# Performance work log

Measured on AMD Instinct MI355X. Metric: run time of the kernel, lower is better.

## Reference

```python
import jax, jax.numpy as jnp
import numpy as np

B, H, L, DM = 16, 8, 512, 512
DK = DM // H  # 64
POW = 2


def setup_inputs() -> dict:
    rng = jax.random.key(0)
    ks = jax.random.split(rng, 16)
    s = 0.05
    d = {
        "query": jax.random.normal(ks[0], (B, L, DM), jnp.float32),
        "key": jax.random.normal(ks[1], (B, L, DM), jnp.float32),
        "value": jax.random.normal(ks[2], (B, L, DM), jnp.float32),
        # torch nn.Linear weights: [out_features, in_features]
        "Wq": jax.random.normal(ks[3], (DM, DM), jnp.float32) * s,
        "bq": jax.random.normal(ks[4], (DM,), jnp.float32) * s,
        "Wk": jax.random.normal(ks[5], (DM, DM), jnp.float32) * s,
        "bk": jax.random.normal(ks[6], (DM,), jnp.float32) * s,
        "Wv": jax.random.normal(ks[7], (DM, DM), jnp.float32) * s,
        "bv": jax.random.normal(ks[8], (DM,), jnp.float32) * s,
        # FCgamma: d_k -> 2 (LrMo == 2)
        "Wg": jax.random.normal(ks[9], (2, DK), jnp.float32) * s,
        "bg": jnp.full((2,), 0.05, jnp.float32),
        "lam1": jnp.zeros((1,), jnp.float32),
        "Wo": jax.random.normal(ks[10], (DM, DM), jnp.float32) * s,
        "bo": jax.random.normal(ks[11], (DM,), jnp.float32) * s,
    }
    return d


def reference(query, key, value, Wq, bq, Wk, bk, Wv, bv, Wg, bg, lam1, Wo, bo):
    def proj(x, W, b):
        # (B,L,DM) -> (B,H,L,DK)
        return (x @ W.T + b).reshape(B, L, H, DK).transpose(0, 2, 1, 3)

    q = proj(query, Wq, bq)
    k = proj(key, Wk, bk)
    v = proj(value, Wv, bv)

    # NOTE: original code overwrites the scaled scores with unscaled QK^T
    scores = jnp.einsum('bhqd,bhkd->bhqk', q, k)  # [B,H,L,L]
    attn = jax.nn.softmax(scores, axis=-1)

    # LrMo == 2: per-row gammas from FCgamma(q) -> 2 channels
    g = q @ Wg.T + bg                      # [B,H,L,2]
    qp = (jnp.abs(g) + 1.0) ** (-POW)      # (|g|+1)^(-pow)

    t = jnp.arange(L, dtype=jnp.float32)
    dist = -0.5 * (t[:, None] - t[None, :]) ** 2   # dist[i,j] = -(i-j)^2/2
    tril = jnp.tril(dist, -1)
    triu = jnp.triu(dist, 0)
    # diag_embed(v) @ M == row-scaling v[i]*M[i,:]
    adj = jnp.exp(qp[..., 1][..., None] * tril + qp[..., 0][..., None] * triu)

    # max-normalize rows of attn
    attn = attn / jnp.max(attn, axis=-1, keepdims=True)
    # sigmoid-gated mix with distance adjacency
    sg = jax.nn.sigmoid(lam1)  # shape (1,)
    attn = sg * attn + (1.0 - sg) * adj
    # degree (row-sum) normalization, non-symmetric
    attn = attn / (jnp.sum(attn, axis=-1, keepdims=True) + 1e-9)

    out = jnp.einsum('bhqk,bhkd->bhqd', attn, v)
    out = out.transpose(0, 2, 1, 3).reshape(B, L, DM)
    return out @ Wo.T + bo
```

## Files before the change

kernel.cpp:

```cpp
#include <hip/hip_runtime.h>
#include <hip/hip_fp16.h>
#include <math.h>

#define B_  16
#define H_  8
#define L_  512
#define DM_ 512
#define DK_ 64
#define LOG2E_ 1.44269504088896340736f
#define NLOG2E_H_ 0.72134752044f

typedef _Float16 f16;
typedef __attribute__((ext_vector_type(2)))  __fp16   fp16v2;
typedef __attribute__((ext_vector_type(8)))  _Float16 f16x8;
typedef __attribute__((ext_vector_type(16))) float f32x16;

__device__ __forceinline__ unsigned pkrtz(float a, float b) {
    union { fp16v2 v; unsigned u; } cv;
    cv.v = __builtin_amdgcn_cvt_pkrtz(a, b);
    return cv.u;
}
__device__ __forceinline__ void plswap(unsigned &x, unsigned &y) {
    asm("v_permlane32_swap_b32 %0, %1" : "+v"(x), "+v"(y));
}

__global__ __launch_bounds__(256) void convw_pack(
    const float* __restrict__ Wq, const float* __restrict__ Wk,
    const float* __restrict__ Wv, const float* __restrict__ Wo,
    f16* __restrict__ Wpk)
{
    const float* src[4] = {Wq, Wk, Wv, Wo};
    const int t = blockIdx.x * 256 + threadIdx.x;
    const int m    = t >> 15;
    const int r    = t & 32767;
    const int lane = r & 31;
    const int hf   = (r >> 5) & 1;
    const int ks   = (r >> 6) & 31;
    const int nb   = r >> 11;
    const float* p = src[m] + (size_t)(nb * 32 + lane) * 512 + ks * 16 + hf * 8;
    float4 x0 = *(const float4*)(p);
    float4 x1 = *(const float4*)(p + 4);
    uint4 v;
    v.x = pkrtz(x0.x, x0.y); v.y = pkrtz(x0.z, x0.w);
    v.z = pkrtz(x1.x, x1.y); v.w = pkrtz(x1.z, x1.w);
    *(uint4*)&Wpk[(size_t)m * 262144 + (size_t)r * 8] = v;
}

template<int XF16, int OUTF32, int TRANSOUT, int NWAVES, int NT>
__device__ __forceinline__ void gemm_stream_core(
    const void* __restrict__ Xv, const f16* __restrict__ Wpk_m,
    const float* __restrict__ bias, void* __restrict__ Yv,
    int row0, int col0, f16* Xl)
{
    const int tid   = threadIdx.x;
    const int w     = tid >> 6;
    const int lane  = tid & 63;
    const int lq    = lane & 31;
    const int half_ = lane >> 5;
    const int colw  = col0 + w * (NT * 32);

    {
        constexpr int TPR = NWAVES * 64 / 32;
        constexpr int FPT = 512 / TPR;
        const int r = tid / TPR, s = tid % TPR;
        const unsigned swz = (r & 7) << 4;
        if (XF16) {
            const f16* X = (const f16*)Xv + (size_t)(row0 + r) * 512 + s * FPT;
            #pragma unroll
            for (int j = 0; j < FPT / 8; ++j) {
                uint4 v = *(const uint4*)(X + j * 8);
                *(uint4*)((char*)Xl + ((r * 1024 + s * FPT * 2 + j * 16) ^ swz)) = v;
            }
        } else {
            const float* X = (const float*)Xv + (size_t)(row0 + r) * 512 + s * FPT;
            #pragma unroll
            for (int j = 0; j < FPT / 8; ++j) {
                float4 x0 = *(const float4*)(X + j * 8);
                float4 x1 = *(const float4*)(X + j * 8 + 4);
                uint4 v;
                v.x = pkrtz(x0.x, x0.y); v.y = pkrtz(x0.z, x0.w);
                v.z = pkrtz(x1.x, x1.y); v.w = pkrtz(x1.z, x1.w);
                *(uint4*)((char*)Xl + ((r * 1024 + s * FPT * 2 + j * 16) ^ swz)) = v;
            }
        }
    }
    __syncthreads();

    f32x16 acc[NT];
    #pragma unroll
    for (int nt = 0; nt < NT; ++nt)
        #pragma unroll
        for (int i = 0; i < 16; ++i) acc[nt][i] = 0.f;

    const f16* wp[NT];
    #pragma unroll
    for (int nt = 0; nt < NT; ++nt)
        wp[nt] = Wpk_m + ((size_t)((colw / 32 + nt) * 64 + half_)) * 256 + lq * 8;

    const unsigned aswz = (lq & 7) << 4;

    #pragma unroll 4
    for (int ks = 0; ks < 32; ++ks) {
        f16x8 a = *(const f16x8*)((char*)Xl + ((lq * 1024 + ks * 32 + half_ * 16) ^ aswz));
        f16x8 bfr[NT];
        #pragma unroll
        for (int nt = 0; nt < NT; ++nt)
            bfr[nt] = *(const f16x8*)(wp[nt] + (size_t)ks * 512);
        #pragma unroll
        for (int nt = 0; nt < NT; ++nt) {
            if (TRANSOUT)
                acc[nt] = __builtin_amdgcn_mfma_f32_32x32x16_f16(bfr[nt], a, acc[nt], 0, 0, 0);
            else
                acc[nt] = __builtin_amdgcn_mfma_f32_32x32x16_f16(a, bfr[nt], acc[nt], 0, 0, 0);
        }
    }

    if (TRANSOUT) {
        const int lg = row0 + lq;
        const int bI = lg >> 9, ll = lg & 511;
        #pragma unroll
        for (int nt = 0; nt < NT; ++nt)
            #pragma unroll
            for (int r = 0; r < 16; ++r) {
                const int n = colw + nt * 32 + (r & 3) + 8 * (r >> 2) + 4 * half_;
                const float v = acc[nt][r] + bias[n];
                ((f16*)Yv)[((size_t)(bI * 512 + n)) * 512 + ll] = (f16)v;
            }
    } else {
        #pragma unroll
        for (int nt = 0; nt < NT; ++nt) {
            const float bv = bias[colw + nt * 32 + lq];
            #pragma unroll
            for (int r = 0; r < 16; ++r) {
                const int row = row0 + (r & 3) + 8 * (r >> 2) + 4 * half_;
                const float v = acc[nt][r] + bv;
                const size_t off = (size_t)row * 512 + colw + nt * 32 + lq;
                if (OUTF32) ((float*)Yv)[off] = v;
                else        ((f16*)Yv)[off]   = (f16)v;
            }
        }
    }
}

__global__ __launch_bounds__(512) void gemm_qkv(
    const float* __restrict__ query, const float* __restrict__ key,
    const float* __restrict__ value, const f16* __restrict__ Wpk,
    const float* __restrict__ bq, const float* __restrict__ bk,
    const float* __restrict__ bv,
    void* __restrict__ Qb, void* __restrict__ Kb, void* __restrict__ VT)
{
    __shared__ f16 Xl[32 * 512];
    const int wg  = blockIdx.x;
    const int xcd = wg & 7;
    const int i   = wg >> 3;
    const int pg  = xcd * 96 + i;
    const int z   = pg >> 8;
    const int y   = pg & 255;
    const int row0 = y * 32;

    if (z == 0)
        gemm_stream_core<0, 0, 0, 8, 2>(query, Wpk,          bq, Qb, row0, 0, Xl);
    else if (z == 1)
        gemm_stream_core<0, 0, 0, 8, 2>(key,   Wpk + 262144, bk, Kb, row0, 0, Xl);
    else
        gemm_stream_core<0, 0, 1, 8, 2>(value, Wpk + 524288, bv, VT, row0, 0, Xl);
}

__global__ __launch_bounds__(256) void gemm_o(
    const void* __restrict__ X, const f16* __restrict__ Wpk,
    const float* __restrict__ bo, void* __restrict__ Y)
{
    __shared__ f16 Xl[32 * 512];
    const int wg  = blockIdx.x;
    const int xcd = wg & 7;
    const int i   = wg >> 3;
    const int pg  = xcd * 64 + i;
    const int cb  = pg & 1;
    const int y   = pg >> 1;
    gemm_stream_core<1, 1, 0, 4, 2>(X, Wpk + 786432, bo, Y, y * 32, cb * 256, Xl);
}

__global__ __launch_bounds__(64) void attn_kernel(
    const f16* __restrict__ Q, const f16* __restrict__ K,
    const f16* __restrict__ VT, const float* __restrict__ Wg,
    const float* __restrict__ bg, const float* __restrict__ lam1,
    f16* __restrict__ ATT)
{
    const int lane = threadIdx.x;
    const int lq   = lane & 31;
    const int half = lane >> 5;
    const int bh   = blockIdx.x;
    const int b    = bh >> 3;
    const int h    = bh & 7;
    const int q0w  = blockIdx.y * 32;
    const int q    = q0w + lq;

    const float sg  = 1.f / (1.f + __expf(-lam1[0]));
    const float osg = 1.f - sg;

    f16x8 qh[4];
    {
        const f16* qrow = Q + ((size_t)(b * L_ + q) * DM_ + h * DK_);
        #pragma unroll
        for (int db = 0; db < 4; ++db)
            qh[db] = *(const f16x8*)&qrow[db * 16 + 8 * half];
    }

    float A0, A1, qpw;
    {
        float g0 = 0.f, g1 = 0.f;
        #pragma unroll
        for (int db = 0; db < 4; ++db)
            #pragma unroll
            for (int j = 0; j < 8; ++j) {
                const int d = db * 16 + 8 * half + j;
                const float qv = (float)qh[db][j];
                g0 = fmaf(qv, Wg[d], g0);
                g1 = fmaf(qv, Wg[64 + d], g1);
            }
        g0 += __shfl_xor(g0, 32);
        g1 += __shfl_xor(g1, 32);
        g0 += bg[0];
        g1 += bg[1];
        const float t0 = fabsf(g0) + 1.f, t1 = fabsf(g1) + 1.f;
        const float p0 = 1.f / (t0 * t0), p1 = 1.f / (t1 * t1);
        A0 = -NLOG2E_H_ * p0;
        A1 = -NLOG2E_H_ * p1;
        float mn = NLOG2E_H_ * fminf(p0, p1);
        #pragma unroll
        for (int off = 1; off < 64; off <<= 1) mn = fminf(mn, __shfl_xor(mn, off));
        qpw = mn;
    }

    f32x16 aS0, aS1, aA0, aA1;
    #pragma unroll
    for (int i = 0; i < 16; ++i) { aS0[i] = 0.f; aS1[i] = 0.f; aA0[i] = 0.f; aA1[i] = 0.f; }
    float m2 = -3.0e38f, sumS = 0.f, sumA = 0.f;

    const f16* Kbase = K  + ((size_t)(b * L_) * DM_ + h * DK_);
    const f16* Vbase = VT + ((size_t)(b * DM_ + h * DK_) * L_);

    for (int t = 0; t < 8; ++t) {
        const int c0 = t * 64;

        f16x8 ka[4], kb2[4], vfa[4], vfb[4];
        #pragma unroll
        for (int db = 0; db < 4; ++db) {
            const int dof = db * 16 + 8 * half;
            ka[db]  = *(const f16x8*)&Kbase[(size_t)(c0 + lq) * DM_ + dof];
            kb2[db] = *(const f16x8*)&Kbase[(size_t)(c0 + 32 + lq) * DM_ + dof];
        }
        #pragma unroll
        for (int ks = 0; ks < 4; ++ks) {
            const int coff = c0 + ks * 16 + 8 * half;
            vfa[ks] = *(const f16x8*)&Vbase[(size_t)lq * L_ + coff];
            vfb[ks] = *(const f16x8*)&Vbase[(size_t)(32 + lq) * L_ + coff];
        }

        f32x16 s2a, s2b;
        #pragma unroll
        for (int i = 0; i < 16; ++i) { s2a[i] = 0.f; s2b[i] = 0.f; }
        #pragma unroll
        for (int db = 0; db < 4; ++db) {
            s2a = __builtin_amdgcn_mfma_f32_32x32x16_f16(ka[db],  qh[db], s2a, 0, 0, 0);
            s2b = __builtin_amdgcn_mfma_f32_32x32x16_f16(kb2[db], qh[db], s2b, 0, 0, 0);
        }

        float tm = s2a[0];
        #pragma unroll
        for (int i = 1; i < 16; ++i) tm = fmaxf(tm, s2a[i]);
        #pragma unroll
        for (int i = 0; i < 16; ++i) tm = fmaxf(tm, s2b[i]);
        tm = fmaxf(tm, __shfl_xor(tm, 32));
        if (__any(tm > m2)) {
            const float nm = fmaxf(m2, tm);
            const float sc = exp2f((m2 - nm) * LOG2E_);
            m2 = nm;
            sumS *= sc;
            #pragma unroll
            for (int r = 0; r < 16; ++r) {
                const float s_ = __shfl(sc, (r & 3) + 8 * (r >> 2) + 4 * half);
                aS0[r] *= s_;
                aS1[r] *= s_;
            }
        }

        const float nmL = m2 * LOG2E_;
        #pragma unroll
        for (int sub = 0; sub < 2; ++sub) {
            const f32x16& s2 = sub ? s2b : s2a;
            #pragma unroll
            for (int ksl = 0; ksl < 2; ++ksl) {
                const int rb = ksl * 8;
                float p[8];
                #pragma unroll
                for (int rr = 0; rr < 8; ++rr) {
                    p[rr] = exp2f(fmaf(s2[rb + rr], LOG2E_, -nmL));
                    sumS += p[rr];
                }
                union { unsigned u[4]; f16x8 v; } f;
                f.u[0] = pkrtz(p[0], p[1]);
                f.u[1] = pkrtz(p[2], p[3]);
                f.u[2] = pkrtz(p[4], p[5]);
                f.u[3] = pkrtz(p[6], p[7]);
                plswap(f.u[0], f.u[2]);
                plswap(f.u[1], f.u[3]);
                const int ks = sub * 2 + ksl;
                aS0 = __builtin_amdgcn_mfma_f32_32x32x16_f16(f.v, vfa[ks], aS0, 0, 0, 0);
                aS1 = __builtin_amdgcn_mfma_f32_32x32x16_f16(f.v, vfb[ks], aS1, 0, 0, 0);
            }
        }

        int gl_ = q0w - (c0 + 63);
        int gh_ = c0 - (q0w + 31);
        int dmin = gl_ > gh_ ? gl_ : gh_;
        if (dmin < 0) dmin = 0;
        if (qpw * (float)(dmin * dmin) < 40.0f) {
            #pragma unroll
            for (int sub = 0; sub < 2; ++sub) {
                #pragma unroll
                for (int ksl = 0; ksl < 2; ++ksl) {
                    float a[8];
                    #pragma unroll
                    for (int rr = 0; rr < 8; ++rr) {
                        const int kk = (rr & 3) + 8 * (rr >> 2) + 16 * ksl + 4 * half;
                        const int diff = q - (c0 + sub * 32 + kk);
                        const float fd = (float)diff;
                        const float coef = diff > 0 ? A1 : A0;
                        a[rr] = exp2f(coef * fd * fd);
                        sumA += a[rr];
                    }
                    union { unsigned u[4]; f16x8 v; } f;
                    f.u[0] = pkrtz(a[0], a[1]);
                    f.u[1] = pkrtz(a[2], a[3]);
                    f.u[2] = pkrtz(a[4], a[5]);
                    f.u[3] = pkrtz(a[6], a[7]);
                    plswap(f.u[0], f.u[2]);
                    plswap(f.u[1], f.u[3]);
                    const int ks = sub * 2 + ksl;
                    aA0 = __builtin_amdgcn_mfma_f32_32x32x16_f16(f.v, vfa[ks], aA0, 0, 0, 0);
                    aA1 = __builtin_amdgcn_mfma_f32_32x32x16_f16(f.v, vfb[ks], aA1, 0, 0, 0);
                }
            }
        }
    }

    const float St = sumS + __shfl_xor(sumS, 32);
    const float At = sumA + __shfl_xor(sumA, 32);
    const float den = sg * St + osg * At + 1e-9f;
    #pragma unroll
    for (int r = 0; r < 16; ++r) {
        const int row = (r & 3) + 8 * (r >> 2) + 4 * half;
        const float dn = __shfl(den, row);
        const float o0 = (sg * aS0[r] + osg * aA0[r]) / dn;
        const float o1 = (sg * aS1[r] + osg * aA1[r]) / dn;
        const size_t base = (size_t)(b * L_ + q0w + row) * DM_ + h * DK_;
        ATT[base + lq]      = (f16)o0;
        ATT[base + 32 + lq] = (f16)o1;
    }
}

extern "C" void kernel_launch(void* const* d_in, const int* in_sizes, int n_in,
                              void* d_out, int out_size, void* d_ws, size_t ws_size,
                              hipStream_t stream)
{
    (void)in_sizes; (void)n_in; (void)out_size; (void)ws_size;
    const float* query = (const float*)d_in[0];
    const float* key   = (const float*)d_in[1];
    const float* value = (const float*)d_in[2];
    const float* Wq = (const float*)d_in[3];  const float* bq = (const float*)d_in[4];
    const float* Wk = (const float*)d_in[5];  const float* bk = (const float*)d_in[6];
    const float* Wv = (const float*)d_in[7];  const float* bv = (const float*)d_in[8];
    const float* Wg = (const float*)d_in[9];  const float* bg = (const float*)d_in[10];
    const float* lam1 = (const float*)d_in[11];
    const float* Wo = (const float*)d_in[12]; const float* bo = (const float*)d_in[13];

    f16* ws16 = (f16*)d_ws;
    const size_t NR = (size_t)B_ * L_ * DM_;
    f16* Kb   = ws16;
    f16* VTb  = ws16 + NR;
    f16* Qb   = ws16 + 2 * NR;
    f16* Wpkb = ws16 + 3 * NR;
    f16* ATTb = Qb;

    convw_pack<<<512, 256, 0, stream>>>(Wq, Wk, Wv, Wo, Wpkb);

    gemm_qkv<<<768, 512, 0, stream>>>(query, key, value, Wpkb, bq, bk, bv,
                                      Qb, Kb, VTb);

    dim3 ga(H_ * B_, L_ / 32);
    attn_kernel<<<ga, 64, 0, stream>>>(Qb, Kb, VTb, Wg, bg, lam1, ATTb);

    gemm_o<<<512, 256, 0, stream>>>(Qb, Wpkb, bo, (float*)d_out);
}
```

Before: 93.42 us.

## Store K and V in MFMA fragment-packed layout per head for coalesced attention loads

```diff
diff --git a/kernel.cpp b/kernel.cpp
--- a/kernel.cpp
+++ b/kernel.cpp
@@ -46,7 +46,7 @@
     *(uint4*)&Wpk[(size_t)m * 262144 + (size_t)r * 8] = v;
 }
 
-template<int XF16, int OUTF32, int TRANSOUT, int NWAVES, int NT>
+template<int XF16, int OUTF32, int OUTMODE, int NWAVES, int NT>
 __device__ __forceinline__ void gemm_stream_core(
     const void* __restrict__ Xv, const f16* __restrict__ Wpk_m,
     const float* __restrict__ bias, void* __restrict__ Yv,
@@ -108,24 +108,47 @@
             bfr[nt] = *(const f16x8*)(wp[nt] + (size_t)ks * 512);
         #pragma unroll
         for (int nt = 0; nt < NT; ++nt) {
-            if (TRANSOUT)
+            if (OUTMODE == 2)
                 acc[nt] = __builtin_amdgcn_mfma_f32_32x32x16_f16(bfr[nt], a, acc[nt], 0, 0, 0);
             else
                 acc[nt] = __builtin_amdgcn_mfma_f32_32x32x16_f16(a, bfr[nt], acc[nt], 0, 0, 0);
         }
     }
 
-    if (TRANSOUT) {
-        const int lg = row0 + lq;
-        const int bI = lg >> 9, ll = lg & 511;
+    if (OUTMODE == 2) {
+        const int b  = row0 >> 9;
+        const int cb = (row0 >> 5) & 15;
+        f16* Kp = (f16*)Yv + (size_t)(b * H_ + w) * 32768;
         #pragma unroll
         for (int nt = 0; nt < NT; ++nt)
             #pragma unroll
-            for (int r = 0; r < 16; ++r) {
-                const int n = colw + nt * 32 + (r & 3) + 8 * (r >> 2) + 4 * half_;
-                const float v = acc[nt][r] + bias[n];
-                ((f16*)Yv)[((size_t)(bI * 512 + n)) * 512 + ll] = (f16)v;
-            }
+            for (int g = 0; g < 4; ++g) {
+                const int n0 = w * 64 + nt * 32 + 8 * g + 4 * half_;
+                const float4 b4 = *(const float4*)&bias[n0];
+                const int ks2 = nt * 2 + (g >> 1);
+                uint2 v;
+                v.x = pkrtz(acc[nt][4 * g + 0] + b4.x, acc[nt][4 * g + 1] + b4.y);
+                v.y = pkrtz(acc[nt][4 * g + 2] + b4.z, acc[nt][4 * g + 3] + b4.w);
+                *(uint2*)&Kp[(cb * 4 + ks2) * 512 + (g & 1) * 256 + lq * 8 + half_ * 4] = v;
+            }
+    } else if (OUTMODE == 1) {
+        const int b  = row0 >> 9;
+        const int cB = row0 & 511;
+        const int tt = cB >> 6;
+        const int kbase = (cB >> 4) & 3;
+        f16* Vp = (f16*)Yv + (size_t)(b * H_ + w) * 32768;
+        #pragma unroll
+        for (int nt = 0; nt < NT; ++nt) {
+            const float bv = bias[w * 64 + nt * 32 + lq];
+            #pragma unroll
+            for (int g = 0; g < 4; ++g) {
+                const int ks2 = kbase + (g >> 1);
+                uint2 v;
+                v.x = pkrtz(acc[nt][4 * g + 0] + bv, acc[nt][4 * g + 1] + bv);
+                v.y = pkrtz(acc[nt][4 * g + 2] + bv, acc[nt][4 * g + 3] + bv);
+                *(uint2*)&Vp[((tt * 4 + ks2) * 2 + nt) * 512 + (g & 1) * 256 + lq * 8 + half_ * 4] = v;
+            }
+        }
     } else {
         #pragma unroll
         for (int nt = 0; nt < NT; ++nt) {
@@ -147,7 +170,7 @@
     const float* __restrict__ value, const f16* __restrict__ Wpk,
     const float* __restrict__ bq, const float* __restrict__ bk,
     const float* __restrict__ bv,
-    void* __restrict__ Qb, void* __restrict__ Kb, void* __restrict__ VT)
+    void* __restrict__ Qb, void* __restrict__ Kpk, void* __restrict__ Vpk)
 {
     __shared__ f16 Xl[32 * 512];
     const int wg  = blockIdx.x;
@@ -159,11 +182,11 @@
     const int row0 = y * 32;
 
     if (z == 0)
-        gemm_stream_core<0, 0, 0, 8, 2>(query, Wpk,          bq, Qb, row0, 0, Xl);
+        gemm_stream_core<0, 0, 0, 8, 2>(query, Wpk,          bq, Qb,  row0, 0, Xl);
     else if (z == 1)
-        gemm_stream_core<0, 0, 0, 8, 2>(key,   Wpk + 262144, bk, Kb, row0, 0, Xl);
+        gemm_stream_core<0, 0, 2, 8, 2>(key,   Wpk + 262144, bk, Kpk, row0, 0, Xl);
     else
-        gemm_stream_core<0, 0, 1, 8, 2>(value, Wpk + 524288, bv, VT, row0, 0, Xl);
+        gemm_stream_core<0, 0, 1, 8, 2>(value, Wpk + 524288, bv, Vpk, row0, 0, Xl);
 }
 
 __global__ __launch_bounds__(256) void gemm_o(
@@ -181,8 +204,8 @@
 }
 
 __global__ __launch_bounds__(64) void attn_kernel(
-    const f16* __restrict__ Q, const f16* __restrict__ K,
-    const f16* __restrict__ VT, const float* __restrict__ Wg,
+    const f16* __restrict__ Q, const f16* __restrict__ Kpk,
+    const f16* __restrict__ Vpk, const float* __restrict__ Wg,
     const float* __restrict__ bg, const float* __restrict__ lam1,
     f16* __restrict__ ATT)
 {
@@ -237,8 +260,9 @@
     for (int i = 0; i < 16; ++i) { aS0[i] = 0.f; aS1[i] = 0.f; aA0[i] = 0.f; aA1[i] = 0.f; }
     float m2 = -3.0e38f, sumS = 0.f, sumA = 0.f;
 
-    const f16* Kbase = K  + ((size_t)(b * L_) * DM_ + h * DK_);
-    const f16* Vbase = VT + ((size_t)(b * DM_ + h * DK_) * L_);
+    const f16* Kp = Kpk + (size_t)(b * H_ + h) * 32768;
+    const f16* Vp = Vpk + (size_t)(b * H_ + h) * 32768;
+    const int  fo = half * 256 + lq * 8;
 
     for (int t = 0; t < 8; ++t) {
         const int c0 = t * 64;
@@ -246,15 +270,13 @@
         f16x8 ka[4], kb2[4], vfa[4], vfb[4];
         #pragma unroll
         for (int db = 0; db < 4; ++db) {
-            const int dof = db * 16 + 8 * half;
-            ka[db]  = *(const f16x8*)&Kbase[(size_t)(c0 + lq) * DM_ + dof];
-            kb2[db] = *(const f16x8*)&Kbase[(size_t)(c0 + 32 + lq) * DM_ + dof];
+            ka[db]  = *(const f16x8*)&Kp[(t * 2 * 4 + db) * 512 + fo];
+            kb2[db] = *(const f16x8*)&Kp[((t * 2 + 1) * 4 + db) * 512 + fo];
         }
         #pragma unroll
         for (int ks = 0; ks < 4; ++ks) {
-            const int coff = c0 + ks * 16 + 8 * half;
-            vfa[ks] = *(const f16x8*)&Vbase[(size_t)lq * L_ + coff];
-            vfb[ks] = *(const f16x8*)&Vbase[(size_t)(32 + lq) * L_ + coff];
+            vfa[ks] = *(const f16x8*)&Vp[((t * 4 + ks) * 2 + 0) * 512 + fo];
+            vfb[ks] = *(const f16x8*)&Vp[((t * 4 + ks) * 2 + 1) * 512 + fo];
         }
 
         f32x16 s2a, s2b;
@@ -377,8 +399,8 @@
 
     f16* ws16 = (f16*)d_ws;
     const size_t NR = (size_t)B_ * L_ * DM_;
-    f16* Kb   = ws16;
-    f16* VTb  = ws16 + NR;
+    f16* Kpkb = ws16;
+    f16* Vpkb = ws16 + NR;
     f16* Qb   = ws16 + 2 * NR;
     f16* Wpkb = ws16 + 3 * NR;
     f16* ATTb = Qb;
@@ -386,10 +408,10 @@
     convw_pack<<<512, 256, 0, stream>>>(Wq, Wk, Wv, Wo, Wpkb);
 
     gemm_qkv<<<768, 512, 0, stream>>>(query, key, value, Wpkb, bq, bk, bv,
-                                      Qb, Kb, VTb);
+                                      Qb, Kpkb, Vpkb);
 
     dim3 ga(H_ * B_, L_ / 32);
-    attn_kernel<<<ga, 64, 0, stream>>>(Qb, Kb, VTb, Wg, bg, lam1, ATTb);
+    attn_kernel<<<ga, 64, 0, stream>>>(Qb, Kpkb, Vpkb, Wg, bg, lam1, ATTb);
 
     gemm_o<<<512, 256, 0, stream>>>(Qb, Wpkb, bo, (float*)d_out);
 }
```

New measurement: 91.31 us. 2.3% less time.
